# Optimization experiments

Hardware: AMD Instinct MI355X
Metric: run time of the kernel (lower is better)

Reference implementation:

```python
import jax, jax.numpy as jnp
import numpy as np

N = 100000
E = 1600000
F_IN = 128
HID = 64
N_CLS = 16


def gcn_conv(x, row, col, W, b, n_nodes):
    # x: [N, Fin]; row/col: [E+N] (self-loops already appended)
    h = x @ W  # [N, Fout]
    ones = jnp.ones(row.shape[0], dtype=x.dtype)
    deg = jax.ops.segment_sum(ones, col, num_segments=n_nodes)  # in-degree incl. self-loop
    dinv = jnp.where(deg > 0, jax.lax.rsqrt(deg), 0.0)
    norm = dinv[row] * dinv[col]  # [E+N]
    msg = h[row] * norm[:, None]  # gather + scale
    out = jax.ops.segment_sum(msg, col, num_segments=n_nodes)  # scatter-add
    return out + b


def setup_inputs() -> dict:
    key = jax.random.key(0)
    k1, k2, k3, k4, k5, k6 = jax.random.split(key, 6)
    x = jax.random.normal(k1, (N, F_IN), dtype=jnp.float32)
    edge_index = jax.random.randint(k2, (2, E), 0, N, dtype=jnp.int64)
    # Glorot-ish init for weights
    W1 = jax.random.normal(k3, (F_IN, HID), dtype=jnp.float32) / np.sqrt(F_IN)
    b1 = jnp.zeros((HID,), dtype=jnp.float32)
    W2 = jax.random.normal(k4, (HID, N_CLS), dtype=jnp.float32) / np.sqrt(HID)
    b2 = jnp.zeros((N_CLS,), dtype=jnp.float32)
    return {"x": x, "edge_index": edge_index, "W1": W1, "b1": b1, "W2": W2, "b2": b2}


def reference(x, edge_index, W1, b1, W2, b2):
    # Add self-loops (GCNConv default add_self_loops=True)
    loop = jnp.arange(N, dtype=edge_index.dtype)
    row = jnp.concatenate([edge_index[0], loop])
    col = jnp.concatenate([edge_index[1], loop])
    h = gcn_conv(x, row, col, W1, b1, N)
    h = jax.nn.relu(h)
    h = gcn_conv(h, row, col, W2, b2, N)
    return jax.nn.log_softmax(h, axis=1)
```

## Files before the change

### kernel.cpp

```cpp
#include <hip/hip_runtime.h>
#include <hip/hip_fp16.h>

#define F_IN 128
#define HID  64
#define NCLS 16
#define NPB  128
#define CAP  4096
#define CHUNK 4096
#define BINTHREADS 1024

typedef _Float16 half_t;
typedef __attribute__((ext_vector_type(8))) _Float16 half8;
typedef __attribute__((ext_vector_type(4))) float float4v;


__global__ __launch_bounds__(BINTHREADS) void phaseA(
    const int* __restrict__ row, const int* __restrict__ col,
    int* __restrict__ cursor, int* __restrict__ ebuf, int E, int NB,
    const float* __restrict__ W1, half_t* __restrict__ W1t, int nblkE)
{
    if ((int)blockIdx.x >= nblkE) {
        for (int i = threadIdx.x; i < F_IN * HID; i += BINTHREADS) {
            int k = i >> 6, n = i & 63;
            W1t[n * F_IN + k] = (half_t)W1[i];
        }
        return;
    }
    __shared__ int hist[1024], base[1024], off[1024];
    for (int i = threadIdx.x; i < NB; i += BINTHREADS) hist[i] = 0;
    int e0 = blockIdx.x * CHUNK + threadIdx.x * 4;
    int nv = min(max(E - e0, 0), 4);
    int4 c4 = make_int4(0, 0, 0, 0), r4 = make_int4(0, 0, 0, 0);
    if (nv == 4) {
        c4 = *(const int4*)&col[e0];
        r4 = *(const int4*)&row[e0];
    } else {
        if (nv > 0) { c4.x = col[e0 + 0]; r4.x = row[e0 + 0]; }
        if (nv > 1) { c4.y = col[e0 + 1]; r4.y = row[e0 + 1]; }
        if (nv > 2) { c4.z = col[e0 + 2]; r4.z = row[e0 + 2]; }
    }
    __syncthreads();
    if (nv > 0) atomicAdd(&hist[c4.x >> 7], 1);
    if (nv > 1) atomicAdd(&hist[c4.y >> 7], 1);
    if (nv > 2) atomicAdd(&hist[c4.z >> 7], 1);
    if (nv > 3) atomicAdd(&hist[c4.w >> 7], 1);
    __syncthreads();
    for (int i = threadIdx.x; i < NB; i += BINTHREADS) {
        int h = hist[i];
        base[i] = h ? (i * CAP + atomicAdd(&cursor[i], h)) : 0;
        off[i] = 0;
    }
    __syncthreads();
    if (nv > 0) { int b = c4.x >> 7; int p = base[b] + atomicAdd(&off[b], 1);
                  if (p < (b + 1) * CAP) ebuf[p] = (r4.x << 7) | (c4.x & (NPB - 1)); }
    if (nv > 1) { int b = c4.y >> 7; int p = base[b] + atomicAdd(&off[b], 1);
                  if (p < (b + 1) * CAP) ebuf[p] = (r4.y << 7) | (c4.y & (NPB - 1)); }
    if (nv > 2) { int b = c4.z >> 7; int p = base[b] + atomicAdd(&off[b], 1);
                  if (p < (b + 1) * CAP) ebuf[p] = (r4.z << 7) | (c4.z & (NPB - 1)); }
    if (nv > 3) { int b = c4.w >> 7; int p = base[b] + atomicAdd(&off[b], 1);
                  if (p < (b + 1) * CAP) ebuf[p] = (r4.w << 7) | (c4.w & (NPB - 1)); }
}


__global__ __launch_bounds__(256) void csr_gemm1(
    const int* __restrict__ ebuf, const int* __restrict__ cursor,
    const float* __restrict__ x, const half_t* __restrict__ W1t,
    int2* __restrict__ rsc, int* __restrict__ csr_row,
    __half* __restrict__ hs1, int N, int NG)
{
    __shared__ int hist[NPB];
    __shared__ float dv[NPB];
    int t = threadIdx.x;

    if ((int)blockIdx.x < NG) {
        int b = blockIdx.x;
        int node0 = b << 7;
        int ebase = b * CAP;
        int p[8];
        #pragma unroll
        for (int k = 0; k < 8; ++k) p[k] = ebuf[ebase + t + 256 * k];
        int cnt = min(cursor[b], CAP);
        if (t < NPB) hist[t] = 0;
        __syncthreads();
        #pragma unroll
        for (int k = 0; k < 8; ++k)
            if (t + 256 * k < cnt) atomicAdd(&hist[p[k] & (NPB - 1)], 1);
        if (cnt > 2048)
            for (int e = 2048 + t; e < cnt; e += 256)
                atomicAdd(&hist[ebuf[ebase + e] & (NPB - 1)], 1);
        __syncthreads();
        if (t < NPB) dv[t] = rsqrtf((float)hist[t] + 1.0f);
        __syncthreads();

        int wv = t >> 6, lane = t & 63;
        int l15 = lane & 15, quad = lane >> 4;
        int mbase = wv * 32;
        int r0 = min(node0 + mbase + l15, N - 1);
        int r1 = min(node0 + mbase + 16 + l15, N - 1);
        const float* x0 = x + (size_t)r0 * F_IN;
        const float* x1 = x + (size_t)r1 * F_IN;
        float4v acc[2][4];
        #pragma unroll
        for (int mt = 0; mt < 2; ++mt)
            #pragma unroll
            for (int j = 0; j < 4; ++j) acc[mt][j] = (float4v){0.f, 0.f, 0.f, 0.f};
        #pragma unroll
        for (int kb = 0; kb < 4; ++kb) {
            int off = kb * 32 + quad * 8;
            float4 fa = *(const float4*)&x0[off];
            float4 fb = *(const float4*)&x0[off + 4];
            float4 ga = *(const float4*)&x1[off];
            float4 gb = *(const float4*)&x1[off + 4];
            half8 a0 = {(half_t)fa.x, (half_t)fa.y, (half_t)fa.z, (half_t)fa.w,
                        (half_t)fb.x, (half_t)fb.y, (half_t)fb.z, (half_t)fb.w};
            half8 a1 = {(half_t)ga.x, (half_t)ga.y, (half_t)ga.z, (half_t)ga.w,
                        (half_t)gb.x, (half_t)gb.y, (half_t)gb.z, (half_t)gb.w};
            #pragma unroll
            for (int j = 0; j < 4; ++j) {
                half8 bv = *(const half8*)&W1t[(size_t)(j * 16 + l15) * F_IN + off];
                acc[0][j] = __builtin_amdgcn_mfma_f32_16x16x32_f16(a0, bv, acc[0][j], 0, 0, 0);
                acc[1][j] = __builtin_amdgcn_mfma_f32_16x16x32_f16(a1, bv, acc[1][j], 0, 0, 0);
            }
        }
        #pragma unroll
        for (int mt = 0; mt < 2; ++mt)
            #pragma unroll
            for (int j = 0; j < 4; ++j)
                #pragma unroll
                for (int r = 0; r < 4; ++r) {
                    int m = mbase + mt * 16 + quad * 4 + r;
                    int n = node0 + m;
                    if (n < N) hs1[(size_t)n * HID + j * 16 + l15] =
                        __float2half(acc[mt][j][r] * dv[m]);
                }
        return;
    }

    __shared__ int cur[NPB];
    __shared__ int wtot;
    int b = blockIdx.x - NG;
    int node0 = b << 7;
    int ebase = b * CAP;
    int p[8];
    #pragma unroll
    for (int k = 0; k < 8; ++k) p[k] = ebuf[ebase + t + 256 * k];
    int cnt = min(cursor[b], CAP);
    if (t < NPB) hist[t] = 0;
    __syncthreads();
    #pragma unroll
    for (int k = 0; k < 8; ++k)
        if (t + 256 * k < cnt) atomicAdd(&hist[p[k] & (NPB - 1)], 1);
    if (cnt > 2048)
        for (int e = 2048 + t; e < cnt; e += 256)
            atomicAdd(&hist[ebuf[ebase + e] & (NPB - 1)], 1);
    __syncthreads();
    int h = 0, incl = 0;
    if (t < NPB) {
        h = hist[t];
        incl = h;
        #pragma unroll
        for (int off = 1; off < 64; off <<= 1) {
            int u = __shfl_up(incl, off, 64);
            if ((t & 63) >= off) incl += u;
        }
        if (t == 63) wtot = incl;
    }
    __syncthreads();
    if (t < NPB) {
        if (t >= 64) incl += wtot;
        int start = ebase + incl - h;
        cur[t] = start;
        int n = node0 + t;
        if (n < N) rsc[n] = make_int2(start, h);
    }
    __syncthreads();
    #pragma unroll
    for (int k = 0; k < 8; ++k)
        if (t + 256 * k < cnt) {
            int pos = atomicAdd(&cur[p[k] & (NPB - 1)], 1);
            csr_row[pos] = p[k] >> 7;
        }
    if (cnt > 2048)
        for (int e = 2048 + t; e < cnt; e += 256) {
            int pp = ebuf[ebase + e];
            int pos = atomicAdd(&cur[pp & (NPB - 1)], 1);
            csr_row[pos] = pp >> 7;
        }
}


__global__ __launch_bounds__(256) void agg_l1(
    const __half* __restrict__ hs1, const int2* __restrict__ rsc,
    const int* __restrict__ csr, const float* __restrict__ b1,
    const float* __restrict__ W2, __half* __restrict__ h2s, int N)
{
    __shared__ float W2l[HID * NCLS];
    __shared__ float o1[32][65];
    for (int i = threadIdx.x; i < HID * NCLS; i += 256) W2l[i] = W2[i];
    __syncthreads();
    int w = threadIdx.x >> 6, lane = threadIdx.x & 63;
    int g = lane >> 3, gl = lane & 7;
    int rowi = w * 8 + g;
    int c = blockIdx.x * 32 + rowi;
    bool active = (c < N);
    int cc = active ? c : 0;
    int2 rc = rsc[cc];
    int e0 = rc.x, e1 = rc.x + rc.y;
    float dc = rsqrtf((float)rc.y + 1.0f);
    const half8* H = (const half8*)hs1;
    half8 sv = H[(size_t)cc * 8 + gl];
    float sum[8];
    #pragma unroll
    for (int k = 0; k < 8; ++k) sum[k] = (float)sv[k];
    int i = e0;
    for (; i + 8 <= e1; i += 8) {
        int id[8];
        #pragma unroll
        for (int s = 0; s < 8; ++s) id[s] = csr[i + s];
        half8 a[8];
        #pragma unroll
        for (int s = 0; s < 8; ++s) a[s] = H[(size_t)id[s] * 8 + gl];
        half8 t0 = a[0] + a[1];
        half8 t1 = a[2] + a[3];
        half8 t2 = a[4] + a[5];
        half8 t3 = a[6] + a[7];
        half8 u0 = t0 + t1;
        half8 u1 = t2 + t3;
        half8 v = u0 + u1;
        #pragma unroll
        for (int k = 0; k < 8; ++k) sum[k] += (float)v[k];
    }
    if (i < e1) {
        int e1m1 = e1 - 1;
        int id[8];
        #pragma unroll
        for (int s = 0; s < 8; ++s) id[s] = csr[min(i + s, e1m1)];
        half8 a[8];
        #pragma unroll
        for (int s = 0; s < 8; ++s) a[s] = H[(size_t)id[s] * 8 + gl];
        #pragma unroll
        for (int s = 0; s < 8; ++s) {
            float fm = (i + s < e1) ? 1.f : 0.f;
            #pragma unroll
            for (int k = 0; k < 8; ++k) sum[k] = fmaf(fm, (float)a[s][k], sum[k]);
        }
    }
    float4 bb0 = *(const float4*)&b1[gl * 8];
    float4 bb1 = *(const float4*)&b1[gl * 8 + 4];
    o1[rowi][gl * 8 + 0] = fmaxf(fmaf(dc, sum[0], bb0.x), 0.f);
    o1[rowi][gl * 8 + 1] = fmaxf(fmaf(dc, sum[1], bb0.y), 0.f);
    o1[rowi][gl * 8 + 2] = fmaxf(fmaf(dc, sum[2], bb0.z), 0.f);
    o1[rowi][gl * 8 + 3] = fmaxf(fmaf(dc, sum[3], bb0.w), 0.f);
    o1[rowi][gl * 8 + 4] = fmaxf(fmaf(dc, sum[4], bb1.x), 0.f);
    o1[rowi][gl * 8 + 5] = fmaxf(fmaf(dc, sum[5], bb1.y), 0.f);
    o1[rowi][gl * 8 + 6] = fmaxf(fmaf(dc, sum[6], bb1.z), 0.f);
    o1[rowi][gl * 8 + 7] = fmaxf(fmaf(dc, sum[7], bb1.w), 0.f);
    int j0 = gl * 2, j1 = gl * 2 + 1;
    float s0 = 0.f, s1 = 0.f;
    const float* orow = o1[rowi];
    #pragma unroll 8
    for (int k = 0; k < HID; ++k) {
        float ov = orow[k];
        s0 = fmaf(ov, W2l[k * NCLS + j0], s0);
        s1 = fmaf(ov, W2l[k * NCLS + j1], s1);
    }
    if (active) {
        __half2 hv;
        hv.x = __float2half(dc * s0);
        hv.y = __float2half(dc * s1);
        ((__half2*)h2s)[(size_t)c * 8 + gl] = hv;
    }
}


__global__ __launch_bounds__(256) void agg2_final(
    const __half* __restrict__ h2s, const int2* __restrict__ rsc,
    const int* __restrict__ csr, const float* __restrict__ b2,
    float* __restrict__ out, int N)
{
    int t = threadIdx.x;
    int w = t >> 6, lane = t & 63;
    int nw = lane >> 1, hl = lane & 1;
    int c = blockIdx.x * 128 + w * 32 + nw;
    bool active = (c < N);
    int cc = active ? c : 0;
    int2 rc = rsc[cc];
    int e0 = rc.x, e1 = rc.x + rc.y;
    float dcv = rsqrtf((float)rc.y + 1.0f);
    const half8* H = (const half8*)h2s;
    half8 sv = H[(size_t)cc * 2 + hl];
    float sum[8];
    #pragma unroll
    for (int k = 0; k < 8; ++k) sum[k] = (float)sv[k];
    int i = e0;
    for (; i + 8 <= e1; i += 8) {
        int id[8];
        #pragma unroll
        for (int s = 0; s < 8; ++s) id[s] = csr[i + s];
        half8 a[8];
        #pragma unroll
        for (int s = 0; s < 8; ++s) a[s] = H[(size_t)id[s] * 2 + hl];
        half8 t0 = a[0] + a[1];
        half8 t1 = a[2] + a[3];
        half8 t2 = a[4] + a[5];
        half8 t3 = a[6] + a[7];
        half8 v = (t0 + t1) + (t2 + t3);
        #pragma unroll
        for (int k = 0; k < 8; ++k) sum[k] += (float)v[k];
    }
    if (i < e1) {
        int e1m1 = e1 - 1;
        int id[8];
        #pragma unroll
        for (int s = 0; s < 8; ++s) id[s] = csr[min(i + s, e1m1)];
        half8 a[8];
        #pragma unroll
        for (int s = 0; s < 8; ++s) a[s] = H[(size_t)id[s] * 2 + hl];
        #pragma unroll
        for (int s = 0; s < 8; ++s) {
            float fm = (i + s < e1) ? 1.f : 0.f;
            #pragma unroll
            for (int k = 0; k < 8; ++k) sum[k] = fmaf(fm, (float)a[s][k], sum[k]);
        }
    }
    float4 bb0 = *(const float4*)&b2[hl * 8];
    float4 bb1 = *(const float4*)&b2[hl * 8 + 4];
    float v0 = fmaf(dcv, sum[0], bb0.x);
    float v1 = fmaf(dcv, sum[1], bb0.y);
    float v2 = fmaf(dcv, sum[2], bb0.z);
    float v3 = fmaf(dcv, sum[3], bb0.w);
    float v4 = fmaf(dcv, sum[4], bb1.x);
    float v5 = fmaf(dcv, sum[5], bb1.y);
    float v6 = fmaf(dcv, sum[6], bb1.z);
    float v7 = fmaf(dcv, sum[7], bb1.w);
    float mx = fmaxf(fmaxf(fmaxf(v0, v1), fmaxf(v2, v3)),
                     fmaxf(fmaxf(v4, v5), fmaxf(v6, v7)));
    mx = fmaxf(mx, __shfl_xor(mx, 1, 64));
    float s = __expf(v0 - mx) + __expf(v1 - mx) + __expf(v2 - mx) + __expf(v3 - mx)
            + __expf(v4 - mx) + __expf(v5 - mx) + __expf(v6 - mx) + __expf(v7 - mx);
    s += __shfl_xor(s, 1, 64);
    float lse = mx + __logf(s);
    if (active) {
        float* o = out + (size_t)c * NCLS + hl * 8;
        *(float4*)&o[0] = make_float4(v0 - lse, v1 - lse, v2 - lse, v3 - lse);
        *(float4*)&o[4] = make_float4(v4 - lse, v5 - lse, v6 - lse, v7 - lse);
    }
}


extern "C" void kernel_launch(void* const* d_in, const int* in_sizes, int n_in,
                              void* d_out, int out_size, void* d_ws, size_t ws_size,
                              hipStream_t stream) {
    const float* x  = (const float*)d_in[0];
    const int*   ei = (const int*)d_in[1];
    const float* W1 = (const float*)d_in[2];
    const float* b1 = (const float*)d_in[3];
    const float* W2 = (const float*)d_in[4];
    const float* b2 = (const float*)d_in[5];
    float* out = (float*)d_out;

    const int N = in_sizes[0] / F_IN;
    const int E = in_sizes[1] / 2;
    const int* row = ei;
    const int* col = ei + E;

    const int NB = (N + NPB - 1) / NPB;
    size_t Np  = ((size_t)N + 15) & ~(size_t)15;
    size_t NBp = ((size_t)NB + 15) & ~(size_t)15;
    size_t Rg  = (size_t)NB * CAP;

    char* p = (char*)d_ws;
    __half* hs1     = (__half*)p;  p += Np * HID * 2;
    __half* h2s     = (__half*)p;  p += Np * NCLS * 2;
    half_t* W1t     = (half_t*)p;  p += (size_t)F_IN * HID * 2;
    int2*   rsc     = (int2*)p;    p += Np * 8;
    int*    csr_row = (int*)p;     p += Rg * 4;
    int*    ebuf    = (int*)p;     p += Rg * 4;
    int*    cursor  = (int*)p;     p += NBp * 4;

    int nblkE = (E + CHUNK - 1) / CHUNK;

    hipMemsetAsync(cursor, 0, NBp * sizeof(int), stream);
    phaseA<<<nblkE + 1, BINTHREADS, 0, stream>>>(row, col, cursor, ebuf, E, NB, W1, W1t, nblkE);
    csr_gemm1<<<2 * NB, 256, 0, stream>>>(ebuf, cursor, x, W1t, rsc, csr_row, hs1, N, NB);
    agg_l1<<<(N + 31) / 32, 256, 0, stream>>>(hs1, rsc, csr_row, b1, W2, h2s, N);
    agg2_final<<<(N + 127) / 128, 256, 0, stream>>>(h2s, rsc, csr_row, b2, out, N);
}
```

Before: 182.0 us.

## Fuse all GCN stages into one persistent kernel with software grid barriers

Replaces the four separate kernel launches with a single persistent kernel whose grid is sized from occupancy. Blocks loop over work items and synchronize between phases with an atomic-counter grid barrier. The binning phase now uses 256-thread blocks that each process 16 edges per thread. The aim is to remove launch gaps and per-kernel tail effects. The cost is that the grid-stride loops reduce per-phase parallelism, the spin barriers add overhead, and correctness relies on every block being co-resident on the device.

```diff
diff --git a/kernel.cpp b/kernel.cpp
--- a/kernel.cpp
+++ b/kernel.cpp
@@ -7,343 +7,384 @@
 #define NPB  128
 #define CAP  4096
 #define CHUNK 4096
-#define BINTHREADS 1024
 
 typedef _Float16 half_t;
 typedef __attribute__((ext_vector_type(8))) _Float16 half8;
 typedef __attribute__((ext_vector_type(4))) float float4v;
 
 
-__global__ __launch_bounds__(BINTHREADS) void phaseA(
+__device__ inline void gridbar(int* cnt, int* gen) {
+    __syncthreads();
+    if (threadIdx.x == 0) {
+        __threadfence();
+        int g = __hip_atomic_load(gen, __ATOMIC_RELAXED, __HIP_MEMORY_SCOPE_AGENT);
+        int n = (int)gridDim.x;
+        if (__hip_atomic_fetch_add(cnt, 1, __ATOMIC_ACQ_REL, __HIP_MEMORY_SCOPE_AGENT) == n - 1) {
+            __hip_atomic_store(cnt, 0, __ATOMIC_RELAXED, __HIP_MEMORY_SCOPE_AGENT);
+            __hip_atomic_fetch_add(gen, 1, __ATOMIC_ACQ_REL, __HIP_MEMORY_SCOPE_AGENT);
+        } else {
+            while (__hip_atomic_load(gen, __ATOMIC_ACQUIRE, __HIP_MEMORY_SCOPE_AGENT) == g)
+                __builtin_amdgcn_s_sleep(8);
+        }
+        __threadfence();
+    }
+    __syncthreads();
+}
+
+
+__global__ __launch_bounds__(256, 4) void fused_gcn(
     const int* __restrict__ row, const int* __restrict__ col,
-    int* __restrict__ cursor, int* __restrict__ ebuf, int E, int NB,
-    const float* __restrict__ W1, half_t* __restrict__ W1t, int nblkE)
+    const float* __restrict__ x, const float* __restrict__ W1,
+    const float* __restrict__ b1, const float* __restrict__ W2,
+    const float* __restrict__ b2, float* __restrict__ out,
+    int* __restrict__ cursor, int* __restrict__ ebuf,
+    half_t* __restrict__ W1t, int2* __restrict__ rsc,
+    int* __restrict__ csr_row, __half* __restrict__ hs1,
+    __half* __restrict__ h2s, int* __restrict__ bar,
+    int N, int E, int NB)
 {
-    if ((int)blockIdx.x >= nblkE) {
-        for (int i = threadIdx.x; i < F_IN * HID; i += BINTHREADS) {
-            int k = i >> 6, n = i & 63;
-            W1t[n * F_IN + k] = (half_t)W1[i];
-        }
-        return;
-    }
-    __shared__ int hist[1024], base[1024], off[1024];
-    for (int i = threadIdx.x; i < NB; i += BINTHREADS) hist[i] = 0;
-    int e0 = blockIdx.x * CHUNK + threadIdx.x * 4;
-    int nv = min(max(E - e0, 0), 4);
-    int4 c4 = make_int4(0, 0, 0, 0), r4 = make_int4(0, 0, 0, 0);
-    if (nv == 4) {
-        c4 = *(const int4*)&col[e0];
-        r4 = *(const int4*)&row[e0];
-    } else {
-        if (nv > 0) { c4.x = col[e0 + 0]; r4.x = row[e0 + 0]; }
-        if (nv > 1) { c4.y = col[e0 + 1]; r4.y = row[e0 + 1]; }
-        if (nv > 2) { c4.z = col[e0 + 2]; r4.z = row[e0 + 2]; }
-    }
-    __syncthreads();
-    if (nv > 0) atomicAdd(&hist[c4.x >> 7], 1);
-    if (nv > 1) atomicAdd(&hist[c4.y >> 7], 1);
-    if (nv > 2) atomicAdd(&hist[c4.z >> 7], 1);
-    if (nv > 3) atomicAdd(&hist[c4.w >> 7], 1);
-    __syncthreads();
-    for (int i = threadIdx.x; i < NB; i += BINTHREADS) {
-        int h = hist[i];
-        base[i] = h ? (i * CAP + atomicAdd(&cursor[i], h)) : 0;
-        off[i] = 0;
-    }
-    __syncthreads();
-    if (nv > 0) { int b = c4.x >> 7; int p = base[b] + atomicAdd(&off[b], 1);
-                  if (p < (b + 1) * CAP) ebuf[p] = (r4.x << 7) | (c4.x & (NPB - 1)); }
-    if (nv > 1) { int b = c4.y >> 7; int p = base[b] + atomicAdd(&off[b], 1);
-                  if (p < (b + 1) * CAP) ebuf[p] = (r4.y << 7) | (c4.y & (NPB - 1)); }
-    if (nv > 2) { int b = c4.z >> 7; int p = base[b] + atomicAdd(&off[b], 1);
-                  if (p < (b + 1) * CAP) ebuf[p] = (r4.z << 7) | (c4.z & (NPB - 1)); }
-    if (nv > 3) { int b = c4.w >> 7; int p = base[b] + atomicAdd(&off[b], 1);
-                  if (p < (b + 1) * CAP) ebuf[p] = (r4.w << 7) | (c4.w & (NPB - 1)); }
-}
-
-
-__global__ __launch_bounds__(256) void csr_gemm1(
-    const int* __restrict__ ebuf, const int* __restrict__ cursor,
-    const float* __restrict__ x, const half_t* __restrict__ W1t,
-    int2* __restrict__ rsc, int* __restrict__ csr_row,
-    __half* __restrict__ hs1, int N, int NG)
-{
-    __shared__ int hist[NPB];
-    __shared__ float dv[NPB];
+    __shared__ char smem[12544];
+    int*   smem_i = (int*)smem;
+    float* smem_f = (float*)smem;
     int t = threadIdx.x;
 
-    if ((int)blockIdx.x < NG) {
-        int b = blockIdx.x;
-        int node0 = b << 7;
-        int ebase = b * CAP;
-        int p[8];
-        #pragma unroll
-        for (int k = 0; k < 8; ++k) p[k] = ebuf[ebase + t + 256 * k];
-        int cnt = min(cursor[b], CAP);
-        if (t < NPB) hist[t] = 0;
-        __syncthreads();
-        #pragma unroll
-        for (int k = 0; k < 8; ++k)
-            if (t + 256 * k < cnt) atomicAdd(&hist[p[k] & (NPB - 1)], 1);
-        if (cnt > 2048)
-            for (int e = 2048 + t; e < cnt; e += 256)
-                atomicAdd(&hist[ebuf[ebase + e] & (NPB - 1)], 1);
-        __syncthreads();
-        if (t < NPB) dv[t] = rsqrtf((float)hist[t] + 1.0f);
-        __syncthreads();
-
-        int wv = t >> 6, lane = t & 63;
-        int l15 = lane & 15, quad = lane >> 4;
-        int mbase = wv * 32;
-        int r0 = min(node0 + mbase + l15, N - 1);
-        int r1 = min(node0 + mbase + 16 + l15, N - 1);
-        const float* x0 = x + (size_t)r0 * F_IN;
-        const float* x1 = x + (size_t)r1 * F_IN;
-        float4v acc[2][4];
-        #pragma unroll
-        for (int mt = 0; mt < 2; ++mt)
-            #pragma unroll
-            for (int j = 0; j < 4; ++j) acc[mt][j] = (float4v){0.f, 0.f, 0.f, 0.f};
-        #pragma unroll
-        for (int kb = 0; kb < 4; ++kb) {
-            int off = kb * 32 + quad * 8;
-            float4 fa = *(const float4*)&x0[off];
-            float4 fb = *(const float4*)&x0[off + 4];
-            float4 ga = *(const float4*)&x1[off];
-            float4 gb = *(const float4*)&x1[off + 4];
-            half8 a0 = {(half_t)fa.x, (half_t)fa.y, (half_t)fa.z, (half_t)fa.w,
-                        (half_t)fb.x, (half_t)fb.y, (half_t)fb.z, (half_t)fb.w};
-            half8 a1 = {(half_t)ga.x, (half_t)ga.y, (half_t)ga.z, (half_t)ga.w,
-                        (half_t)gb.x, (half_t)gb.y, (half_t)gb.z, (half_t)gb.w};
+    {
+        int* histB = smem_i;
+        int* baseB = smem_i + 1024;
+        int* offB  = smem_i + 2048;
+        int nch = (E + CHUNK - 1) / CHUNK;
+        for (int ch = blockIdx.x; ch <= nch; ch += gridDim.x) {
+            if (ch == nch) {
+                for (int i = t; i < F_IN * HID; i += 256) {
+                    int k = i >> 6, n = i & 63;
+                    W1t[n * F_IN + k] = (half_t)W1[i];
+                }
+                continue;
+            }
+            for (int i = t; i < NB; i += 256) histB[i] = 0;
+            int e0 = ch * CHUNK + t * 16;
+            int4 c4[4], r4[4];
+            int nvv[4];
             #pragma unroll
             for (int j = 0; j < 4; ++j) {
-                half8 bv = *(const half8*)&W1t[(size_t)(j * 16 + l15) * F_IN + off];
-                acc[0][j] = __builtin_amdgcn_mfma_f32_16x16x32_f16(a0, bv, acc[0][j], 0, 0, 0);
-                acc[1][j] = __builtin_amdgcn_mfma_f32_16x16x32_f16(a1, bv, acc[1][j], 0, 0, 0);
-            }
+                int ej = e0 + j * 4;
+                int nv = min(max(E - ej, 0), 4);
+                nvv[j] = nv;
+                c4[j] = make_int4(0, 0, 0, 0); r4[j] = make_int4(0, 0, 0, 0);
+                if (nv == 4) {
+                    c4[j] = *(const int4*)&col[ej];
+                    r4[j] = *(const int4*)&row[ej];
+                } else {
+                    if (nv > 0) { c4[j].x = col[ej + 0]; r4[j].x = row[ej + 0]; }
+                    if (nv > 1) { c4[j].y = col[ej + 1]; r4[j].y = row[ej + 1]; }
+                    if (nv > 2) { c4[j].z = col[ej + 2]; r4[j].z = row[ej + 2]; }
+                }
+            }
+            __syncthreads();
+            #pragma unroll
+            for (int j = 0; j < 4; ++j) {
+                if (nvv[j] > 0) atomicAdd(&histB[c4[j].x >> 7], 1);
+                if (nvv[j] > 1) atomicAdd(&histB[c4[j].y >> 7], 1);
+                if (nvv[j] > 2) atomicAdd(&histB[c4[j].z >> 7], 1);
+                if (nvv[j] > 3) atomicAdd(&histB[c4[j].w >> 7], 1);
+            }
+            __syncthreads();
+            for (int i = t; i < NB; i += 256) {
+                int h = histB[i];
+                baseB[i] = h ? (i * CAP + atomicAdd(&cursor[i], h)) : 0;
+                offB[i] = 0;
+            }
+            __syncthreads();
+            #pragma unroll
+            for (int j = 0; j < 4; ++j) {
+                if (nvv[j] > 0) { int b = c4[j].x >> 7; int p = baseB[b] + atomicAdd(&offB[b], 1);
+                                  if (p < (b + 1) * CAP) ebuf[p] = (r4[j].x << 7) | (c4[j].x & (NPB - 1)); }
+                if (nvv[j] > 1) { int b = c4[j].y >> 7; int p = baseB[b] + atomicAdd(&offB[b], 1);
+                                  if (p < (b + 1) * CAP) ebuf[p] = (r4[j].y << 7) | (c4[j].y & (NPB - 1)); }
+                if (nvv[j] > 2) { int b = c4[j].z >> 7; int p = baseB[b] + atomicAdd(&offB[b], 1);
+                                  if (p < (b + 1) * CAP) ebuf[p] = (r4[j].z << 7) | (c4[j].z & (NPB - 1)); }
+                if (nvv[j] > 3) { int b = c4[j].w >> 7; int p = baseB[b] + atomicAdd(&offB[b], 1);
+                                  if (p < (b + 1) * CAP) ebuf[p] = (r4[j].w << 7) | (c4[j].w & (NPB - 1)); }
+            }
+            __syncthreads();
         }
-        #pragma unroll
-        for (int mt = 0; mt < 2; ++mt)
+    }
+    gridbar(bar, bar + 1);
+
+    {
+        int*   hist = smem_i;
+        float* dv   = smem_f + 128;
+        int*   cur  = smem_i + 256;
+        int*   wtot = smem_i + 384;
+        int ntask = 2 * NB;
+        for (int task = blockIdx.x; task < ntask; task += gridDim.x) {
+            __syncthreads();
+            if (task < NB) {
+                int b = task;
+                int node0 = b << 7;
+                int ebase = b * CAP;
+                int p[8];
+                #pragma unroll
+                for (int k = 0; k < 8; ++k) p[k] = ebuf[ebase + t + 256 * k];
+                int cnt = min(cursor[b], CAP);
+                if (t < NPB) hist[t] = 0;
+                __syncthreads();
+                #pragma unroll
+                for (int k = 0; k < 8; ++k)
+                    if (t + 256 * k < cnt) atomicAdd(&hist[p[k] & (NPB - 1)], 1);
+                if (cnt > 2048)
+                    for (int e = 2048 + t; e < cnt; e += 256)
+                        atomicAdd(&hist[ebuf[ebase + e] & (NPB - 1)], 1);
+                __syncthreads();
+                if (t < NPB) dv[t] = rsqrtf((float)hist[t] + 1.0f);
+                __syncthreads();
+
+                int wv = t >> 6, lane = t & 63;
+                int l15 = lane & 15, quad = lane >> 4;
+                int mbase = wv * 32;
+                int r0 = min(node0 + mbase + l15, N - 1);
+                int r1 = min(node0 + mbase + 16 + l15, N - 1);
+                const float* x0 = x + (size_t)r0 * F_IN;
+                const float* x1 = x + (size_t)r1 * F_IN;
+                float4v acc[2][4];
+                #pragma unroll
+                for (int mt = 0; mt < 2; ++mt)
+                    #pragma unroll
+                    for (int j = 0; j < 4; ++j) acc[mt][j] = (float4v){0.f, 0.f, 0.f, 0.f};
+                #pragma unroll
+                for (int kb = 0; kb < 4; ++kb) {
+                    int off = kb * 32 + quad * 8;
+                    float4 fa = *(const float4*)&x0[off];
+                    float4 fb = *(const float4*)&x0[off + 4];
+                    float4 ga = *(const float4*)&x1[off];
+                    float4 gb = *(const float4*)&x1[off + 4];
+                    half8 a0 = {(half_t)fa.x, (half_t)fa.y, (half_t)fa.z, (half_t)fa.w,
+                                (half_t)fb.x, (half_t)fb.y, (half_t)fb.z, (half_t)fb.w};
+                    half8 a1 = {(half_t)ga.x, (half_t)ga.y, (half_t)ga.z, (half_t)ga.w,
+                                (half_t)gb.x, (half_t)gb.y, (half_t)gb.z, (half_t)gb.w};
+                    #pragma unroll
+                    for (int j = 0; j < 4; ++j) {
+                        half8 bv = *(const half8*)&W1t[(size_t)(j * 16 + l15) * F_IN + off];
+                        acc[0][j] = __builtin_amdgcn_mfma_f32_16x16x32_f16(a0, bv, acc[0][j], 0, 0, 0);
+                        acc[1][j] = __builtin_amdgcn_mfma_f32_16x16x32_f16(a1, bv, acc[1][j], 0, 0, 0);
+                    }
+                }
+                #pragma unroll
+                for (int mt = 0; mt < 2; ++mt)
+                    #pragma unroll
+                    for (int j = 0; j < 4; ++j)
+                        #pragma unroll
+                        for (int r = 0; r < 4; ++r) {
+                            int m = mbase + mt * 16 + quad * 4 + r;
+                            int n = node0 + m;
+                            if (n < N) hs1[(size_t)n * HID + j * 16 + l15] =
+                                __float2half(acc[mt][j][r] * dv[m]);
+                        }
+            } else {
+                int b = task - NB;
+                int node0 = b << 7;
+                int ebase = b * CAP;
+                int p[8];
+                #pragma unroll
+                for (int k = 0; k < 8; ++k) p[k] = ebuf[ebase + t + 256 * k];
+                int cnt = min(cursor[b], CAP);
+                if (t < NPB) hist[t] = 0;
+                __syncthreads();
+                #pragma unroll
+                for (int k = 0; k < 8; ++k)
+                    if (t + 256 * k < cnt) atomicAdd(&hist[p[k] & (NPB - 1)], 1);
+                if (cnt > 2048)
+                    for (int e = 2048 + t; e < cnt; e += 256)
+                        atomicAdd(&hist[ebuf[ebase + e] & (NPB - 1)], 1);
+                __syncthreads();
+                int h = 0, incl = 0;
+                if (t < NPB) {
+                    h = hist[t];
+                    incl = h;
+                    #pragma unroll
+                    for (int off = 1; off < 64; off <<= 1) {
+                        int u = __shfl_up(incl, off, 64);
+                        if ((t & 63) >= off) incl += u;
+                    }
+                    if (t == 63) *wtot = incl;
+                }
+                __syncthreads();
+                if (t < NPB) {
+                    if (t >= 64) incl += *wtot;
+                    int start = ebase + incl - h;
+                    cur[t] = start;
+                    int n = node0 + t;
+                    if (n < N) rsc[n] = make_int2(start, h);
+                }
+                __syncthreads();
+                #pragma unroll
+                for (int k = 0; k < 8; ++k)
+                    if (t + 256 * k < cnt) {
+                        int pos = atomicAdd(&cur[p[k] & (NPB - 1)], 1);
+                        csr_row[pos] = p[k] >> 7;
+                    }
+                if (cnt > 2048)
+                    for (int e = 2048 + t; e < cnt; e += 256) {
+                        int pp = ebuf[ebase + e];
+                        int pos = atomicAdd(&cur[pp & (NPB - 1)], 1);
+                        csr_row[pos] = pp >> 7;
+                    }
+            }
+        }
+    }
+    gridbar(bar, bar + 1);
+
+    {
+        float* W2l = smem_f;
+        float* o1  = smem_f + 1024;
+        for (int i = t; i < HID * NCLS; i += 256) W2l[i] = W2[i];
+        __syncthreads();
+        int w = t >> 6, lane = t & 63;
+        int g = lane >> 3, gl = lane & 7;
+        int rowi = w * 8 + g;
+        float* orow = o1 + rowi * 65;
+        const half8* H = (const half8*)hs1;
+        int nt3 = (N + 31) >> 5;
+        for (int vb = blockIdx.x; vb < nt3; vb += gridDim.x) {
+            int c = vb * 32 + rowi;
+            bool active = (c < N);
+            int cc = active ? c : 0;
+            int2 rc = rsc[cc];
+            int e0 = rc.x, e1 = rc.x + rc.y;
+            float dc = rsqrtf((float)rc.y + 1.0f);
+            half8 sv = H[(size_t)cc * 8 + gl];
+            float sum[8];
             #pragma unroll
-            for (int j = 0; j < 4; ++j)
-                #pragma unroll
-                for (int r = 0; r < 4; ++r) {
-                    int m = mbase + mt * 16 + quad * 4 + r;
-                    int n = node0 + m;
-                    if (n < N) hs1[(size_t)n * HID + j * 16 + l15] =
-                        __float2half(acc[mt][j][r] * dv[m]);
-                }
-        return;
-    }
-
-    __shared__ int cur[NPB];
-    __shared__ int wtot;
-    int b = blockIdx.x - NG;
-    int node0 = b << 7;
-    int ebase = b * CAP;
-    int p[8];
-    #pragma unroll
-    for (int k = 0; k < 8; ++k) p[k] = ebuf[ebase + t + 256 * k];
-    int cnt = min(cursor[b], CAP);
-    if (t < NPB) hist[t] = 0;
-    __syncthreads();
-    #pragma unroll
-    for (int k = 0; k < 8; ++k)
-        if (t + 256 * k < cnt) atomicAdd(&hist[p[k] & (NPB - 1)], 1);
-    if (cnt > 2048)
-        for (int e = 2048 + t; e < cnt; e += 256)
-            atomicAdd(&hist[ebuf[ebase + e] & (NPB - 1)], 1);
-    __syncthreads();
-    int h = 0, incl = 0;
-    if (t < NPB) {
-        h = hist[t];
-        incl = h;
-        #pragma unroll
-        for (int off = 1; off < 64; off <<= 1) {
-            int u = __shfl_up(incl, off, 64);
-            if ((t & 63) >= off) incl += u;
+            for (int k = 0; k < 8; ++k) sum[k] = (float)sv[k];
+            int i = e0;
+            for (; i + 8 <= e1; i += 8) {
+                int id[8];
+                #pragma unroll
+                for (int s = 0; s < 8; ++s) id[s] = csr_row[i + s];
+                half8 a[8];
+                #pragma unroll
+                for (int s = 0; s < 8; ++s) a[s] = H[(size_t)id[s] * 8 + gl];
+                half8 t0 = a[0] + a[1];
+                half8 t1 = a[2] + a[3];
+                half8 t2 = a[4] + a[5];
+                half8 t3 = a[6] + a[7];
+                half8 v = (t0 + t1) + (t2 + t3);
+                #pragma unroll
+                for (int k = 0; k < 8; ++k) sum[k] += (float)v[k];
+            }
+            if (i < e1) {
+                int e1m1 = e1 - 1;
+                int id[8];
+                #pragma unroll
+                for (int s = 0; s < 8; ++s) id[s] = csr_row[min(i + s, e1m1)];
+                half8 a[8];
+                #pragma unroll
+                for (int s = 0; s < 8; ++s) a[s] = H[(size_t)id[s] * 8 + gl];
+                #pragma unroll
+                for (int s = 0; s < 8; ++s) {
+                    float fm = (i + s < e1) ? 1.f : 0.f;
+                    #pragma unroll
+                    for (int k = 0; k < 8; ++k) sum[k] = fmaf(fm, (float)a[s][k], sum[k]);
+                }
+            }
+            float4 bb0 = *(const float4*)&b1[gl * 8];
+            float4 bb1 = *(const float4*)&b1[gl * 8 + 4];
+            orow[gl * 8 + 0] = fmaxf(fmaf(dc, sum[0], bb0.x), 0.f);
+            orow[gl * 8 + 1] = fmaxf(fmaf(dc, sum[1], bb0.y), 0.f);
+            orow[gl * 8 + 2] = fmaxf(fmaf(dc, sum[2], bb0.z), 0.f);
+            orow[gl * 8 + 3] = fmaxf(fmaf(dc, sum[3], bb0.w), 0.f);
+            orow[gl * 8 + 4] = fmaxf(fmaf(dc, sum[4], bb1.x), 0.f);
+            orow[gl * 8 + 5] = fmaxf(fmaf(dc, sum[5], bb1.y), 0.f);
+            orow[gl * 8 + 6] = fmaxf(fmaf(dc, sum[6], bb1.z), 0.f);
+            orow[gl * 8 + 7] = fmaxf(fmaf(dc, sum[7], bb1.w), 0.f);
+            int j0 = gl * 2, j1 = gl * 2 + 1;
+            float s0 = 0.f, s1 = 0.f;
+            #pragma unroll 8
+            for (int k = 0; k < HID; ++k) {
+                float ov = orow[k];
+                s0 = fmaf(ov, W2l[k * NCLS + j0], s0);
+                s1 = fmaf(ov, W2l[k * NCLS + j1], s1);
+            }
+            if (active) {
+                __half2 hv;
+                hv.x = __float2half(dc * s0);
+                hv.y = __float2half(dc * s1);
+                ((__half2*)h2s)[(size_t)c * 8 + gl] = hv;
+            }
         }
-        if (t == 63) wtot = incl;
-    }
-    __syncthreads();
-    if (t < NPB) {
-        if (t >= 64) incl += wtot;
-        int start = ebase + incl - h;
-        cur[t] = start;
-        int n = node0 + t;
-        if (n < N) rsc[n] = make_int2(start, h);
-    }
-    __syncthreads();
-    #pragma unroll
-    for (int k = 0; k < 8; ++k)
-        if (t + 256 * k < cnt) {
-            int pos = atomicAdd(&cur[p[k] & (NPB - 1)], 1);
-            csr_row[pos] = p[k] >> 7;
+    }
+    gridbar(bar, bar + 1);
+
+    {
+        int w = t >> 6, lane = t & 63;
+        int nw = lane >> 1, hl = lane & 1;
+        const half8* H = (const half8*)h2s;
+        float4 bb0 = *(const float4*)&b2[hl * 8];
+        float4 bb1 = *(const float4*)&b2[hl * 8 + 4];
+        int nt4 = (N + 127) >> 7;
+        for (int vb = blockIdx.x; vb < nt4; vb += gridDim.x) {
+            int c = vb * 128 + w * 32 + nw;
+            bool active = (c < N);
+            int cc = active ? c : 0;
+            int2 rc = rsc[cc];
+            int e0 = rc.x, e1 = rc.x + rc.y;
+            float dcv = rsqrtf((float)rc.y + 1.0f);
+            half8 sv = H[(size_t)cc * 2 + hl];
+            float sum[8];
+            #pragma unroll
+            for (int k = 0; k < 8; ++k) sum[k] = (float)sv[k];
+            int i = e0;
+            for (; i + 8 <= e1; i += 8) {
+                int id[8];
+                #pragma unroll
+                for (int s = 0; s < 8; ++s) id[s] = csr_row[i + s];
+                half8 a[8];
+                #pragma unroll
+                for (int s = 0; s < 8; ++s) a[s] = H[(size_t)id[s] * 2 + hl];
+                half8 t0 = a[0] + a[1];
+                half8 t1 = a[2] + a[3];
+                half8 t2 = a[4] + a[5];
+                half8 t3 = a[6] + a[7];
+                half8 v = (t0 + t1) + (t2 + t3);
+                #pragma unroll
+                for (int k = 0; k < 8; ++k) sum[k] += (float)v[k];
+            }
+            if (i < e1) {
+                int e1m1 = e1 - 1;
+                int id[8];
+                #pragma unroll
+                for (int s = 0; s < 8; ++s) id[s] = csr_row[min(i + s, e1m1)];
+                half8 a[8];
+                #pragma unroll
+                for (int s = 0; s < 8; ++s) a[s] = H[(size_t)id[s] * 2 + hl];
+                #pragma unroll
+                for (int s = 0; s < 8; ++s) {
+                    float fm = (i + s < e1) ? 1.f : 0.f;
+                    #pragma unroll
+                    for (int k = 0; k < 8; ++k) sum[k] = fmaf(fm, (float)a[s][k], sum[k]);
+                }
+            }
+            float v0 = fmaf(dcv, sum[0], bb0.x);
+            float v1 = fmaf(dcv, sum[1], bb0.y);
+            float v2 = fmaf(dcv, sum[2], bb0.z);
+            float v3 = fmaf(dcv, sum[3], bb0.w);
+            float v4 = fmaf(dcv, sum[4], bb1.x);
+            float v5 = fmaf(dcv, sum[5], bb1.y);
+            float v6 = fmaf(dcv, sum[6], bb1.z);
+            float v7 = fmaf(dcv, sum[7], bb1.w);
+            float mx = fmaxf(fmaxf(fmaxf(v0, v1), fmaxf(v2, v3)),
+                             fmaxf(fmaxf(v4, v5), fmaxf(v6, v7)));
+            mx = fmaxf(mx, __shfl_xor(mx, 1, 64));
+            float s = __expf(v0 - mx) + __expf(v1 - mx) + __expf(v2 - mx) + __expf(v3 - mx)
+                    + __expf(v4 - mx) + __expf(v5 - mx) + __expf(v6 - mx) + __expf(v7 - mx);
+            s += __shfl_xor(s, 1, 64);
+            float lse = mx + __logf(s);
+            if (active) {
+                float* o = out + (size_t)c * NCLS + hl * 8;
+                *(float4*)&o[0] = make_float4(v0 - lse, v1 - lse, v2 - lse, v3 - lse);
+                *(float4*)&o[4] = make_float4(v4 - lse, v5 - lse, v6 - lse, v7 - lse);
+            }
         }
-    if (cnt > 2048)
-        for (int e = 2048 + t; e < cnt; e += 256) {
-            int pp = ebuf[ebase + e];
-            int pos = atomicAdd(&cur[pp & (NPB - 1)], 1);
-            csr_row[pos] = pp >> 7;
-        }
-}
-
-
-__global__ __launch_bounds__(256) void agg_l1(
-    const __half* __restrict__ hs1, const int2* __restrict__ rsc,
-    const int* __restrict__ csr, const float* __restrict__ b1,
-    const float* __restrict__ W2, __half* __restrict__ h2s, int N)
-{
-    __shared__ float W2l[HID * NCLS];
-    __shared__ float o1[32][65];
-    for (int i = threadIdx.x; i < HID * NCLS; i += 256) W2l[i] = W2[i];
-    __syncthreads();
-    int w = threadIdx.x >> 6, lane = threadIdx.x & 63;
-    int g = lane >> 3, gl = lane & 7;
-    int rowi = w * 8 + g;
-    int c = blockIdx.x * 32 + rowi;
-    bool active = (c < N);
-    int cc = active ? c : 0;
-    int2 rc = rsc[cc];
-    int e0 = rc.x, e1 = rc.x + rc.y;
-    float dc = rsqrtf((float)rc.y + 1.0f);
-    const half8* H = (const half8*)hs1;
-    half8 sv = H[(size_t)cc * 8 + gl];
-    float sum[8];
-    #pragma unroll
-    for (int k = 0; k < 8; ++k) sum[k] = (float)sv[k];
-    int i = e0;
-    for (; i + 8 <= e1; i += 8) {
-        int id[8];
-        #pragma unroll
-        for (int s = 0; s < 8; ++s) id[s] = csr[i + s];
-        half8 a[8];
-        #pragma unroll
-        for (int s = 0; s < 8; ++s) a[s] = H[(size_t)id[s] * 8 + gl];
-        half8 t0 = a[0] + a[1];
-        half8 t1 = a[2] + a[3];
-        half8 t2 = a[4] + a[5];
-        half8 t3 = a[6] + a[7];
-        half8 u0 = t0 + t1;
-        half8 u1 = t2 + t3;
-        half8 v = u0 + u1;
-        #pragma unroll
-        for (int k = 0; k < 8; ++k) sum[k] += (float)v[k];
-    }
-    if (i < e1) {
-        int e1m1 = e1 - 1;
-        int id[8];
-        #pragma unroll
-        for (int s = 0; s < 8; ++s) id[s] = csr[min(i + s, e1m1)];
-        half8 a[8];
-        #pragma unroll
-        for (int s = 0; s < 8; ++s) a[s] = H[(size_t)id[s] * 8 + gl];
-        #pragma unroll
-        for (int s = 0; s < 8; ++s) {
-            float fm = (i + s < e1) ? 1.f : 0.f;
-            #pragma unroll
-            for (int k = 0; k < 8; ++k) sum[k] = fmaf(fm, (float)a[s][k], sum[k]);
-        }
-    }
-    float4 bb0 = *(const float4*)&b1[gl * 8];
-    float4 bb1 = *(const float4*)&b1[gl * 8 + 4];
-    o1[rowi][gl * 8 + 0] = fmaxf(fmaf(dc, sum[0], bb0.x), 0.f);
-    o1[rowi][gl * 8 + 1] = fmaxf(fmaf(dc, sum[1], bb0.y), 0.f);
-    o1[rowi][gl * 8 + 2] = fmaxf(fmaf(dc, sum[2], bb0.z), 0.f);
-    o1[rowi][gl * 8 + 3] = fmaxf(fmaf(dc, sum[3], bb0.w), 0.f);
-    o1[rowi][gl * 8 + 4] = fmaxf(fmaf(dc, sum[4], bb1.x), 0.f);
-    o1[rowi][gl * 8 + 5] = fmaxf(fmaf(dc, sum[5], bb1.y), 0.f);
-    o1[rowi][gl * 8 + 6] = fmaxf(fmaf(dc, sum[6], bb1.z), 0.f);
-    o1[rowi][gl * 8 + 7] = fmaxf(fmaf(dc, sum[7], bb1.w), 0.f);
-    int j0 = gl * 2, j1 = gl * 2 + 1;
-    float s0 = 0.f, s1 = 0.f;
-    const float* orow = o1[rowi];
-    #pragma unroll 8
-    for (int k = 0; k < HID; ++k) {
-        float ov = orow[k];
-        s0 = fmaf(ov, W2l[k * NCLS + j0], s0);
-        s1 = fmaf(ov, W2l[k * NCLS + j1], s1);
-    }
-    if (active) {
-        __half2 hv;
-        hv.x = __float2half(dc * s0);
-        hv.y = __float2half(dc * s1);
-        ((__half2*)h2s)[(size_t)c * 8 + gl] = hv;
-    }
-}
-
-
-__global__ __launch_bounds__(256) void agg2_final(
-    const __half* __restrict__ h2s, const int2* __restrict__ rsc,
-    const int* __restrict__ csr, const float* __restrict__ b2,
-    float* __restrict__ out, int N)
-{
-    int t = threadIdx.x;
-    int w = t >> 6, lane = t & 63;
-    int nw = lane >> 1, hl = lane & 1;
-    int c = blockIdx.x * 128 + w * 32 + nw;
-    bool active = (c < N);
-    int cc = active ? c : 0;
-    int2 rc = rsc[cc];
-    int e0 = rc.x, e1 = rc.x + rc.y;
-    float dcv = rsqrtf((float)rc.y + 1.0f);
-    const half8* H = (const half8*)h2s;
-    half8 sv = H[(size_t)cc * 2 + hl];
-    float sum[8];
-    #pragma unroll
-    for (int k = 0; k < 8; ++k) sum[k] = (float)sv[k];
-    int i = e0;
-    for (; i + 8 <= e1; i += 8) {
-        int id[8];
-        #pragma unroll
-        for (int s = 0; s < 8; ++s) id[s] = csr[i + s];
-        half8 a[8];
-        #pragma unroll
-        for (int s = 0; s < 8; ++s) a[s] = H[(size_t)id[s] * 2 + hl];
-        half8 t0 = a[0] + a[1];
-        half8 t1 = a[2] + a[3];
-        half8 t2 = a[4] + a[5];
-        half8 t3 = a[6] + a[7];
-        half8 v = (t0 + t1) + (t2 + t3);
-        #pragma unroll
-        for (int k = 0; k < 8; ++k) sum[k] += (float)v[k];
-    }
-    if (i < e1) {
-        int e1m1 = e1 - 1;
-        int id[8];
-        #pragma unroll
-        for (int s = 0; s < 8; ++s) id[s] = csr[min(i + s, e1m1)];
-        half8 a[8];
-        #pragma unroll
-        for (int s = 0; s < 8; ++s) a[s] = H[(size_t)id[s] * 2 + hl];
-        #pragma unroll
-        for (int s = 0; s < 8; ++s) {
-            float fm = (i + s < e1) ? 1.f : 0.f;
-            #pragma unroll
-            for (int k = 0; k < 8; ++k) sum[k] = fmaf(fm, (float)a[s][k], sum[k]);
-        }
-    }
-    float4 bb0 = *(const float4*)&b2[hl * 8];
-    float4 bb1 = *(const float4*)&b2[hl * 8 + 4];
-    float v0 = fmaf(dcv, sum[0], bb0.x);
-    float v1 = fmaf(dcv, sum[1], bb0.y);
-    float v2 = fmaf(dcv, sum[2], bb0.z);
-    float v3 = fmaf(dcv, sum[3], bb0.w);
-    float v4 = fmaf(dcv, sum[4], bb1.x);
-    float v5 = fmaf(dcv, sum[5], bb1.y);
-    float v6 = fmaf(dcv, sum[6], bb1.z);
-    float v7 = fmaf(dcv, sum[7], bb1.w);
-    float mx = fmaxf(fmaxf(fmaxf(v0, v1), fmaxf(v2, v3)),
-                     fmaxf(fmaxf(v4, v5), fmaxf(v6, v7)));
-    mx = fmaxf(mx, __shfl_xor(mx, 1, 64));
-    float s = __expf(v0 - mx) + __expf(v1 - mx) + __expf(v2 - mx) + __expf(v3 - mx)
-            + __expf(v4 - mx) + __expf(v5 - mx) + __expf(v6 - mx) + __expf(v7 - mx);
-    s += __shfl_xor(s, 1, 64);
-    float lse = mx + __logf(s);
-    if (active) {
-        float* o = out + (size_t)c * NCLS + hl * 8;
-        *(float4*)&o[0] = make_float4(v0 - lse, v1 - lse, v2 - lse, v3 - lse);
-        *(float4*)&o[4] = make_float4(v4 - lse, v5 - lse, v6 - lse, v7 - lse);
     }
 }
 
@@ -377,12 +418,25 @@
     int*    csr_row = (int*)p;     p += Rg * 4;
     int*    ebuf    = (int*)p;     p += Rg * 4;
     int*    cursor  = (int*)p;     p += NBp * 4;
-
-    int nblkE = (E + CHUNK - 1) / CHUNK;
-
-    hipMemsetAsync(cursor, 0, NBp * sizeof(int), stream);
-    phaseA<<<nblkE + 1, BINTHREADS, 0, stream>>>(row, col, cursor, ebuf, E, NB, W1, W1t, nblkE);
-    csr_gemm1<<<2 * NB, 256, 0, stream>>>(ebuf, cursor, x, W1t, rsc, csr_row, hs1, N, NB);
-    agg_l1<<<(N + 31) / 32, 256, 0, stream>>>(hs1, rsc, csr_row, b1, W2, h2s, N);
-    agg2_final<<<(N + 127) / 128, 256, 0, stream>>>(h2s, rsc, csr_row, b2, out, N);
+    int*    bar     = (int*)p;     p += 64;
+
+    static int s_grid = 0;
+    if (!s_grid) {
+        int dev = 0;
+        hipGetDevice(&dev);
+        hipDeviceProp_t prop;
+        int ncu = 256;
+        if (hipGetDeviceProperties(&prop, dev) == hipSuccess) ncu = prop.multiProcessorCount;
+        int perCU = 0;
+        if (hipOccupancyMaxActiveBlocksPerMultiprocessor(&perCU, fused_gcn, 256, 0) != hipSuccess || perCU < 1)
+            perCU = 2;
+        long cap = (long)ncu * perCU;
+        s_grid = (int)(cap < 1024 ? cap : 1024);
+        if (s_grid < 1) s_grid = 1;
+    }
+
+    hipMemsetAsync(cursor, 0, NBp * sizeof(int) + 64, stream);
+    fused_gcn<<<s_grid, 256, 0, stream>>>(row, col, x, W1, b1, W2, b2, out,
+                                          cursor, ebuf, W1t, rsc, csr_row,
+                                          hs1, h2s, bar, N, E, NB);
 }
```

Result: slower. 598.2 us (+228.7%).
